# Optimization experiments

Measured on AMD Instinct MI355X. Metric: run time of the kernel, lower is better.

## Reference

```python
import jax, jax.numpy as jnp
import numpy as np

# --- configuration (mirrors init_kwargs) ---
N_G = (256, 256, 128, 128)   # tem.hyper['n_g'] per-module sizes
N_ACTIONS = 4                 # tem action space
NUM_STATES = 4096
BATCH = 16384
G_TOTAL = sum(N_G)            # 768


def setup_inputs() -> dict:
    key = jax.random.key(0)
    ks = jax.random.split(key, 4 + len(N_G))
    inp = {
        "current_state_index": jax.random.randint(ks[0], (BATCH,), 0, NUM_STATES),
        "action_index": jax.random.randint(ks[1], (BATCH,), 0, N_ACTIONS),
        # xavier-ish init scale for embedding / classifier
        "emb": jax.random.normal(ks[2], (NUM_STATES, G_TOTAL), jnp.float32) * 0.02,
        "W_cls": jax.random.normal(ks[3], (NUM_STATES, G_TOTAL), jnp.float32) * 0.02,
        "b_cls": jnp.zeros((NUM_STATES,), jnp.float32),
    }
    # per-module bank of action-conditioned transition matrices D_a: [n_actions, n_g_f, n_g_f]
    for f, n in enumerate(N_G):
        inp[f"D{f}"] = jax.random.normal(ks[4 + f], (N_ACTIONS, n, n), jnp.float32) * (1.0 / np.sqrt(n))
    return inp


def _transition(g_f, D_f, onehot):
    # Routed action-conditioned transition (replaces the CPU per-action loop):
    # delta[b, j] = sum_i D_f[a_b, j, i] * g_f[b, i], dispatched via one-hot over actions.
    delta = jnp.einsum('aji,bi,ba->bj', D_f, g_f, onehot)
    # TEM generative clamp activation f_g_clamp
    return jnp.clip(g_f + delta, -1.0, 1.0)


def reference(current_state_index, action_index, emb, D0, D1, D2, D3, W_cls, b_cls):
    g_flat = emb[current_state_index]                                   # [B, G_TOTAL]
    onehot = jax.nn.one_hot(action_index, N_ACTIONS, dtype=g_flat.dtype)  # [B, A]
    # _split_g: slice flat grid code into TEM modules
    g_mods = jnp.split(g_flat, np.cumsum(np.array(N_G))[:-1].tolist(), axis=1)
    Ds = (D0, D1, D2, D3)
    g_next = [_transition(g_f, D_f, onehot) for g_f, D_f in zip(g_mods, Ds)]
    g_next_flat = jnp.concatenate(g_next, axis=1)                       # [B, G_TOTAL]
    logits = g_next_flat @ W_cls.T + b_cls                              # [B, NUM_STATES]
    return logits, g_next_flat
```

## Files before the change

kernel.cpp:

```cpp
#include <hip/hip_runtime.h>
#include <hip/hip_bf16.h>
#include <stdint.h>


typedef __attribute__((ext_vector_type(8))) short short8;
typedef __attribute__((ext_vector_type(4))) float floatx4;

__device__ __forceinline__ float bf2f(short s) {
    unsigned int u = ((unsigned int)(unsigned short)s) << 16;
    float f;
    __builtin_memcpy(&f, &u, 4);
    return f;
}
__device__ __forceinline__ short f2bf(float f) {
    unsigned int u;
    __builtin_memcpy(&u, &f, 4);
    u = (u + 0x7FFFu + ((u >> 16) & 1u)) >> 16;
    return (short)u;
}

#define GLLDS16(g, l)                                                                     \
    __builtin_amdgcn_global_load_lds((const __attribute__((address_space(1))) void*)(g),  \
                                     (__attribute__((address_space(3))) void*)(l), 16, 0, 0)

#define ROWS_PAD 16896

__global__ __launch_bounds__(1024) void setup_kernel(const int* __restrict__ act,
                                                     int* __restrict__ meta,
                                                     int* __restrict__ s2o) {
    const int tid = threadIdx.x;
    const int lane = tid & 63;
    const int w = tid >> 6;
    __shared__ int lc[16][4];
    int c0 = 0, c1 = 0, c2 = 0, c3 = 0;
    for (int i = tid; i < 16384; i += 1024) {
        int a = act[i];
        unsigned long long m0 = __ballot(a == 0);
        unsigned long long m1 = __ballot(a == 1);
        unsigned long long m2 = __ballot(a == 2);
        unsigned long long m3 = __ballot(a == 3);
        if (lane == 0) {
            c0 += __popcll(m0); c1 += __popcll(m1);
            c2 += __popcll(m2); c3 += __popcll(m3);
        }
    }
    if (lane == 0) { lc[w][0] = c0; lc[w][1] = c1; lc[w][2] = c2; lc[w][3] = c3; }
    for (int i = tid; i < ROWS_PAD; i += 1024) s2o[i] = -1;
    __syncthreads();
    if (tid == 0) {
        int base = 0;
        for (int k = 0; k < 4; ++k) {
            int c = 0;
            for (int ww = 0; ww < 16; ++ww) c += lc[ww][k];
            meta[4 + k] = base;
            meta[9 + k] = base;
            base += (c + 127) & ~127;
        }
        meta[8] = base;
    }
}

__global__ __launch_bounds__(256) void assign_kernel(const int* __restrict__ act,
                                                     int* __restrict__ meta,
                                                     int* __restrict__ slot_of,
                                                     int* __restrict__ s2o) {
    const int row = blockIdx.x * 256 + threadIdx.x;
    const int lane = threadIdx.x & 63;
    const int a = act[row];
    const unsigned long long lt = (1ull << lane) - 1ull;
    int* cursor = meta + 9;
    int slot = 0;
    #pragma unroll
    for (int k = 0; k < 4; ++k) {
        unsigned long long m = __ballot(a == k);
        int c = __popcll(m);
        int gb = 0;
        if (lane == 0 && c) gb = atomicAdd(&cursor[k], c);
        gb = __shfl(gb, 0);
        if (a == k) slot = gb + __popcll(m & lt);
    }
    slot_of[row] = slot;
    s2o[slot] = row;
}

__global__ __launch_bounds__(256) void prep_kernel(
    const int* __restrict__ state, const int* __restrict__ slot_of,
    const float* __restrict__ emb, const float* __restrict__ W,
    const float* __restrict__ D0, const float* __restrict__ D1,
    const float* __restrict__ D2, const float* __restrict__ D3,
    short* __restrict__ A1, short* __restrict__ Wb, short* __restrict__ Db) {
    long e = (long)blockIdx.x * 256 + threadIdx.x;
    const float* src;
    short* dst;
    long di;
    if (e < 3145728L) {
        int b = (int)(e / 192);
        int cc = (int)(e % 192);
        int s = state[b];
        int d = slot_of[b];
        src = emb + (long)s * 768 + cc * 4;
        dst = A1; di = (long)d * 192 + cc;
    } else if (e < 3932160L) {
        long t = e - 3145728L;
        src = W + t * 4; dst = Wb; di = t;
    } else if (e < 3997696L) {
        long t = e - 3932160L;
        src = D0 + t * 4; dst = Db; di = t;
    } else if (e < 4063232L) {
        long t = e - 3997696L;
        src = D1 + t * 4; dst = Db + 262144; di = t;
    } else if (e < 4079616L) {
        long t = e - 4063232L;
        src = D2 + t * 4; dst = Db + 524288; di = t;
    } else {
        long t = e - 4079616L;
        src = D3 + t * 4; dst = Db + 589824; di = t;
    }
    float4 v = *(const float4*)src;
    union { ushort4 u4; short s4[4]; } o;
    o.s4[0] = f2bf(v.x); o.s4[1] = f2bf(v.y);
    o.s4[2] = f2bf(v.z); o.s4[3] = f2bf(v.w);
    *(ushort4*)(dst + di * 4) = o.u4;
}

__global__ __launch_bounds__(256) void trans_gemm_kernel(
    const short* __restrict__ A, const short* __restrict__ Db,
    const int* __restrict__ meta, const int* __restrict__ s2o,
    float* __restrict__ gnext, short* __restrict__ A2) {
    __shared__ short Ash[128 * 64];
    __shared__ short Bsh[128 * 64];
    const int bx = blockIdx.x, bm = blockIdx.y;
    int n, bn, coloff;
    long Doff;
    if (bx < 4) {
        n = 256; bn = bx & 1;
        int f = bx >> 1;
        coloff = f * 256; Doff = (long)f * 262144;
    } else {
        n = 128; bn = 0;
        int f = bx - 4;
        coloff = 512 + f * 128; Doff = 524288 + (long)f * 65536;
    }
    const int rowbase = bm * 128;
    const int sb4 = meta[8];
    if (rowbase >= sb4) return;
    const int a = (rowbase >= meta[5]) + (rowbase >= meta[6]) + (rowbase >= meta[7]);
    const short* Bm = Db + Doff + (long)a * n * n;

    const int tid = threadIdx.x;
    const int lane = tid & 63;
    const int w = tid >> 6;
    const int wm = w & 1, wn = w >> 1;
    const long arow0 = (long)rowbase;
    const long brow0 = (long)bn * 128;
    const int lrow = lane & 15;
    const int q = lane >> 4;

    floatx4 acc[4][4] = {};

    for (int k0 = 0; k0 < n; k0 += 64) {
        #pragma unroll
        for (int it = 0; it < 4; ++it) {
            int c = it * 256 + tid;
            int r = c >> 3, cc = c & 7;
            int gc = cc ^ (r & 7);
            GLLDS16(A + (arow0 + r) * 768 + coloff + k0 + gc * 8, &Ash[c * 8]);
            GLLDS16(Bm + (brow0 + r) * n + k0 + gc * 8, &Bsh[c * 8]);
        }
        __syncthreads();
        #pragma unroll
        for (int kk = 0; kk < 2; ++kk) {
            short8 af[4], bv[4];
            #pragma unroll
            for (int mi = 0; mi < 4; ++mi) {
                int rr = wm * 64 + mi * 16 + lrow;
                int ch = (kk * 4 + q) ^ (rr & 7);
                af[mi] = *(const short8*)&Ash[rr * 64 + ch * 8];
            }
            #pragma unroll
            for (int ni = 0; ni < 4; ++ni) {
                int rr = wn * 64 + ni * 16 + lrow;
                int ch = (kk * 4 + q) ^ (rr & 7);
                bv[ni] = *(const short8*)&Bsh[rr * 64 + ch * 8];
            }
            #pragma unroll
            for (int mi = 0; mi < 4; ++mi)
                #pragma unroll
                for (int ni = 0; ni < 4; ++ni)
                    acc[mi][ni] = __builtin_amdgcn_mfma_f32_16x16x32_bf16(
                        af[mi], bv[ni], acc[mi][ni], 0, 0, 0);
        }
        __syncthreads();
    }

    const int jb = bn * 128 + wn * 64;
    const int rowb2 = rowbase + wm * 64;
    #pragma unroll
    for (int mi = 0; mi < 4; ++mi) {
        #pragma unroll
        for (int r = 0; r < 4; ++r) {
            int srow = rowb2 + mi * 16 + q * 4 + r;
            int orig = s2o[srow];
            if (orig >= 0) {
                #pragma unroll
                for (int ni = 0; ni < 4; ++ni) {
                    int jl = jb + ni * 16 + lrow;
                    long sidx = (long)srow * 768 + coloff + jl;
                    long oidx = (long)orig * 768 + coloff + jl;
                    float g = bf2f(A[sidx]);
                    float v = g + acc[mi][ni][r];
                    v = fminf(1.0f, fmaxf(-1.0f, v));
                    gnext[oidx] = v;
                    A2[oidx] = f2bf(v);
                }
            }
        }
    }
}

__global__ __launch_bounds__(512) void cls_gemm_kernel(
    const short* __restrict__ A, const short* __restrict__ Bm,
    const float* __restrict__ bias, float* __restrict__ out) {
    __shared__ short lds[4][2][8192];

    int lin = blockIdx.y * 16 + blockIdx.x;
    lin = (lin & 7) * 128 + (lin >> 3);
    const int bn = lin & 15, bm = lin >> 4;

    const int tid = threadIdx.x;
    const int lane = tid & 63;
    const int w = tid >> 6;
    const int wm = w & 1, wn = w >> 1;
    const long arow0 = (long)bm * 256;
    const long brow0 = (long)bn * 256;
    const int lrow = lane & 15;
    const int q = lane >> 4;

    floatx4 acc[8][4] = {};

    auto STAGE = [&](int t, int b) {
        const int k0 = t * 32;
        #pragma unroll
        for (int it = 0; it < 2; ++it) {
            int c = it * 512 + tid;
            int r = c >> 2, s = c & 3;
            int gc = s ^ ((r >> 1) & 3);
            GLLDS16(A + (arow0 + r) * 768 + k0 + gc * 8, &lds[b][0][c * 8]);
            GLLDS16(Bm + (brow0 + r) * 768 + k0 + gc * 8, &lds[b][1][c * 8]);
        }
    };

    auto COMPUTE = [&](int b) {
        const short* Ab = lds[b][0];
        const short* Bb = lds[b][1];
        short8 af[8], bv[4];
        #pragma unroll
        for (int mi = 0; mi < 8; ++mi) {
            int rr = wm * 128 + mi * 16 + lrow;
            int sl = q ^ ((rr >> 1) & 3);
            af[mi] = *(const short8*)&Ab[rr * 32 + sl * 8];
        }
        #pragma unroll
        for (int ni = 0; ni < 4; ++ni) {
            int rr = wn * 64 + ni * 16 + lrow;
            int sl = q ^ ((rr >> 1) & 3);
            bv[ni] = *(const short8*)&Bb[rr * 32 + sl * 8];
        }
        __builtin_amdgcn_s_setprio(1);
        #pragma unroll
        for (int mi = 0; mi < 8; ++mi)
            #pragma unroll
            for (int ni = 0; ni < 4; ++ni)
                acc[mi][ni] = __builtin_amdgcn_mfma_f32_16x16x32_bf16(
                    af[mi], bv[ni], acc[mi][ni], 0, 0, 0);
        __builtin_amdgcn_s_setprio(0);
    };

    STAGE(0, 0); STAGE(1, 1); STAGE(2, 2);

    for (int t = 0; t < 22; ++t) {
        asm volatile("s_waitcnt vmcnt(8)" ::: "memory");
        __builtin_amdgcn_s_barrier();
        if (t < 21) STAGE(t + 3, (t + 3) & 3);
        COMPUTE(t & 3);
    }
    asm volatile("s_waitcnt vmcnt(4)" ::: "memory");
    __builtin_amdgcn_s_barrier();
    COMPUTE(22 & 3);
    asm volatile("s_waitcnt vmcnt(0)" ::: "memory");
    __builtin_amdgcn_s_barrier();
    COMPUTE(23 & 3);

    const int rowb2 = bm * 256 + wm * 128;
    const int colbase = bn * 256 + wn * 64;
    #pragma unroll
    for (int mi = 0; mi < 8; ++mi) {
        #pragma unroll
        for (int r = 0; r < 4; ++r) {
            int row = rowb2 + mi * 16 + q * 4 + r;
            #pragma unroll
            for (int ni = 0; ni < 4; ++ni) {
                int col = colbase + ni * 16 + lrow;
                out[(long)row * 4096 + col] = acc[mi][ni][r] + bias[col];
            }
        }
    }
}

extern "C" void kernel_launch(void* const* d_in, const int* in_sizes, int n_in,
                              void* d_out, int out_size, void* d_ws, size_t ws_size,
                              hipStream_t stream) {
    const int* state  = (const int*)d_in[0];
    const int* act    = (const int*)d_in[1];
    const float* emb  = (const float*)d_in[2];
    const float* W    = (const float*)d_in[3];
    const float* bias = (const float*)d_in[4];
    const float* D0   = (const float*)d_in[5];
    const float* D1   = (const float*)d_in[6];
    const float* D2   = (const float*)d_in[7];
    const float* D3   = (const float*)d_in[8];

    float* logits = (float*)d_out;
    float* gnext  = logits + 67108864L;

    short* A1 = (short*)d_ws;
    short* A2 = A1 + 12976128L;
    short* Wb = A2 + 12976128L;
    short* Db = Wb + 3145728L;
    int* meta    = (int*)(Db + 655360);
    int* slot_of = meta + 16;
    int* s2o     = slot_of + 16384;

    setup_kernel<<<1, 1024, 0, stream>>>(act, meta, s2o);
    assign_kernel<<<64, 256, 0, stream>>>(act, meta, slot_of, s2o);
    prep_kernel<<<16000, 256, 0, stream>>>(state, slot_of, emb, W, D0, D1, D2, D3,
                                           A1, Wb, Db);
    trans_gemm_kernel<<<dim3(6, 132), 256, 0, stream>>>(A1, Db, meta, s2o, gnext, A2);
    cls_gemm_kernel<<<dim3(16, 64), 512, 0, stream>>>(A2, Wb, bias, logits);
}
```

Measured before the change: 489.2 us.

## Merge sort setup kernels and multi-buffer transition GEMM with async LDS prefetch

Merges the setup and assign kernels into one single-block sort kernel that uses LDS cursors instead of global atomics, removing one launch. The transition GEMM drops its two-barrier K-loop with 64-wide tiles and uses a 4-stage ring of 32-wide LDS buffers. It prefetches three tiles ahead with global_load_lds, waits with explicit vmcnt and raises priority around the MFMA block. This aims to overlap global loads with MFMA compute and cut barrier stalls. The trade-offs are a serial single-block assignment pass and hand-written waitcnt counts that must match the number of issued loads.

```diff
diff --git a/kernel.cpp b/kernel.cpp
--- a/kernel.cpp
+++ b/kernel.cpp
@@ -25,13 +25,15 @@
 
 #define ROWS_PAD 16896
 
-__global__ __launch_bounds__(1024) void setup_kernel(const int* __restrict__ act,
-                                                     int* __restrict__ meta,
-                                                     int* __restrict__ s2o) {
+__global__ __launch_bounds__(1024) void sort_kernel(const int* __restrict__ act,
+                                                    int* __restrict__ meta,
+                                                    int* __restrict__ slot_of,
+                                                    int* __restrict__ s2o) {
     const int tid = threadIdx.x;
     const int lane = tid & 63;
     const int w = tid >> 6;
     __shared__ int lc[16][4];
+    __shared__ int cur[4];
     int c0 = 0, c1 = 0, c2 = 0, c3 = 0;
     for (int i = tid; i < 16384; i += 1024) {
         int a = act[i];
@@ -53,34 +55,28 @@
             int c = 0;
             for (int ww = 0; ww < 16; ++ww) c += lc[ww][k];
             meta[4 + k] = base;
-            meta[9 + k] = base;
+            cur[k] = base;
             base += (c + 127) & ~127;
         }
         meta[8] = base;
     }
-}
-
-__global__ __launch_bounds__(256) void assign_kernel(const int* __restrict__ act,
-                                                     int* __restrict__ meta,
-                                                     int* __restrict__ slot_of,
-                                                     int* __restrict__ s2o) {
-    const int row = blockIdx.x * 256 + threadIdx.x;
-    const int lane = threadIdx.x & 63;
-    const int a = act[row];
+    __syncthreads();
     const unsigned long long lt = (1ull << lane) - 1ull;
-    int* cursor = meta + 9;
-    int slot = 0;
-    #pragma unroll
-    for (int k = 0; k < 4; ++k) {
-        unsigned long long m = __ballot(a == k);
-        int c = __popcll(m);
-        int gb = 0;
-        if (lane == 0 && c) gb = atomicAdd(&cursor[k], c);
-        gb = __shfl(gb, 0);
-        if (a == k) slot = gb + __popcll(m & lt);
-    }
-    slot_of[row] = slot;
-    s2o[slot] = row;
+    for (int i = tid; i < 16384; i += 1024) {
+        int a = act[i];
+        int slot = 0;
+        #pragma unroll
+        for (int k = 0; k < 4; ++k) {
+            unsigned long long m = __ballot(a == k);
+            int c = __popcll(m);
+            int gb = 0;
+            if (lane == 0 && c) gb = atomicAdd(&cur[k], c);
+            gb = __shfl(gb, 0);
+            if (a == k) slot = gb + __popcll(m & lt);
+        }
+        slot_of[i] = slot;
+        s2o[slot] = i;
+    }
 }
 
 __global__ __launch_bounds__(256) void prep_kernel(
@@ -127,8 +123,7 @@
     const short* __restrict__ A, const short* __restrict__ Db,
     const int* __restrict__ meta, const int* __restrict__ s2o,
     float* __restrict__ gnext, short* __restrict__ A2) {
-    __shared__ short Ash[128 * 64];
-    __shared__ short Bsh[128 * 64];
+    __shared__ short lds[4][2][4096];
     const int bx = blockIdx.x, bm = blockIdx.y;
     int n, bn, coloff;
     long Doff;
@@ -142,8 +137,7 @@
         coloff = 512 + f * 128; Doff = 524288 + (long)f * 65536;
     }
     const int rowbase = bm * 128;
-    const int sb4 = meta[8];
-    if (rowbase >= sb4) return;
+    if (rowbase >= meta[8]) return;
     const int a = (rowbase >= meta[5]) + (rowbase >= meta[6]) + (rowbase >= meta[7]);
     const short* Bm = Db + Doff + (long)a * n * n;
 
@@ -155,43 +149,62 @@
     const long brow0 = (long)bn * 128;
     const int lrow = lane & 15;
     const int q = lane >> 4;
+    const int NT = n >> 5;
 
     floatx4 acc[4][4] = {};
 
-    for (int k0 = 0; k0 < n; k0 += 64) {
-        #pragma unroll
-        for (int it = 0; it < 4; ++it) {
+    auto STAGE = [&](int t, int b) {
+        const int k0 = t * 32;
+        #pragma unroll
+        for (int it = 0; it < 2; ++it) {
             int c = it * 256 + tid;
-            int r = c >> 3, cc = c & 7;
-            int gc = cc ^ (r & 7);
-            GLLDS16(A + (arow0 + r) * 768 + coloff + k0 + gc * 8, &Ash[c * 8]);
-            GLLDS16(Bm + (brow0 + r) * n + k0 + gc * 8, &Bsh[c * 8]);
-        }
-        __syncthreads();
-        #pragma unroll
-        for (int kk = 0; kk < 2; ++kk) {
-            short8 af[4], bv[4];
+            int r = c >> 2, s = c & 3;
+            int gc = s ^ ((r >> 1) & 3);
+            GLLDS16(A + (arow0 + r) * 768 + coloff + k0 + gc * 8, &lds[b][0][c * 8]);
+            GLLDS16(Bm + (brow0 + r) * (long)n + k0 + gc * 8, &lds[b][1][c * 8]);
+        }
+    };
+
+    auto COMPUTE = [&](int b) {
+        const short* Ab = lds[b][0];
+        const short* Bb = lds[b][1];
+        short8 af[4], bv[4];
+        #pragma unroll
+        for (int mi = 0; mi < 4; ++mi) {
+            int rr = wm * 64 + mi * 16 + lrow;
+            int sl = q ^ ((rr >> 1) & 3);
+            af[mi] = *(const short8*)&Ab[rr * 32 + sl * 8];
+        }
+        #pragma unroll
+        for (int ni = 0; ni < 4; ++ni) {
+            int rr = wn * 64 + ni * 16 + lrow;
+            int sl = q ^ ((rr >> 1) & 3);
+            bv[ni] = *(const short8*)&Bb[rr * 32 + sl * 8];
+        }
+        __builtin_amdgcn_s_setprio(1);
+        #pragma unroll
+        for (int mi = 0; mi < 4; ++mi)
             #pragma unroll
-            for (int mi = 0; mi < 4; ++mi) {
-                int rr = wm * 64 + mi * 16 + lrow;
-                int ch = (kk * 4 + q) ^ (rr & 7);
-                af[mi] = *(const short8*)&Ash[rr * 64 + ch * 8];
-            }
-            #pragma unroll
-            for (int ni = 0; ni < 4; ++ni) {
-                int rr = wn * 64 + ni * 16 + lrow;
-                int ch = (kk * 4 + q) ^ (rr & 7);
-                bv[ni] = *(const short8*)&Bsh[rr * 64 + ch * 8];
-            }
-            #pragma unroll
-            for (int mi = 0; mi < 4; ++mi)
-                #pragma unroll
-                for (int ni = 0; ni < 4; ++ni)
-                    acc[mi][ni] = __builtin_amdgcn_mfma_f32_16x16x32_bf16(
-                        af[mi], bv[ni], acc[mi][ni], 0, 0, 0);
-        }
-        __syncthreads();
-    }
+            for (int ni = 0; ni < 4; ++ni)
+                acc[mi][ni] = __builtin_amdgcn_mfma_f32_16x16x32_bf16(
+                    af[mi], bv[ni], acc[mi][ni], 0, 0, 0);
+        __builtin_amdgcn_s_setprio(0);
+    };
+
+    STAGE(0, 0); STAGE(1, 1); STAGE(2, 2);
+
+    for (int t = 0; t < NT - 2; ++t) {
+        asm volatile("s_waitcnt vmcnt(8)" ::: "memory");
+        __builtin_amdgcn_s_barrier();
+        if (t + 3 < NT) STAGE(t + 3, (t + 3) & 3);
+        COMPUTE(t & 3);
+    }
+    asm volatile("s_waitcnt vmcnt(4)" ::: "memory");
+    __builtin_amdgcn_s_barrier();
+    COMPUTE((NT - 2) & 3);
+    asm volatile("s_waitcnt vmcnt(0)" ::: "memory");
+    __builtin_amdgcn_s_barrier();
+    COMPUTE((NT - 1) & 3);
 
     const int jb = bn * 128 + wn * 64;
     const int rowb2 = rowbase + wm * 64;
@@ -331,8 +344,7 @@
     int* slot_of = meta + 16;
     int* s2o     = slot_of + 16384;
 
-    setup_kernel<<<1, 1024, 0, stream>>>(act, meta, s2o);
-    assign_kernel<<<64, 256, 0, stream>>>(act, meta, slot_of, s2o);
+    sort_kernel<<<1, 1024, 0, stream>>>(act, meta, slot_of, s2o);
     prep_kernel<<<16000, 256, 0, stream>>>(state, slot_of, emb, W, D0, D1, D2, D3,
                                            A1, Wb, Db);
     trans_gemm_kernel<<<dim3(6, 132), 256, 0, stream>>>(A1, Db, meta, s2o, gnext, A2);
```

New measurement: 486.6 us. Within noise of the previous version (-0.5%).
